# Kernel tuning notes

Hardware: AMD Instinct MI355X
Metric: run time of the kernel (lower is better)

Reference implementation:

```python
import jax, jax.numpy as jnp
import numpy as np

B, K = 16384, 32      # batch nodes, sampled neighbors per node
N, F, E = 1000000, 128, 128  # table size, feature_dim, embed_dim


def setup_inputs() -> dict:
    key = jax.random.key(0)
    k1, k2, k3 = jax.random.split(key, 3)
    id2feat = jax.random.normal(k1, (N, F), dtype=jnp.float32)
    # xavier_uniform for weight
    limit = float(np.sqrt(6.0 / (F + E)))
    weight = jax.random.uniform(k2, (F, E), dtype=jnp.float32, minval=-limit, maxval=limit)
    bias = jnp.zeros((E,), dtype=jnp.float32)
    neigh_idx = jax.random.randint(k3, (B, K), 0, N, dtype=jnp.int64)
    return {"id2feat": id2feat, "weight": weight, "bias": bias, "neigh_idx": neigh_idx}


def reference(id2feat, weight, bias, neigh_idx):
    # gather neighbor features: [B, K, F]
    feats = id2feat[neigh_idx]
    # linear transform then mean over neighbors (== mask.mm(embed_matrix))
    emb = jnp.einsum('bkf,fe->bke', feats, weight) + bias  # [B, K, E]
    return emb.mean(axis=1)  # [B, E]
```

## Files before the change

### kernel.cpp

```cpp
#include <hip/hip_runtime.h>


#define BATCH 16384
#define KNB   32
#define FDIM  128
#define EDIM  128
#define ROWS_PER_BLOCK 16
#define IDX_PITCH 33
#define A_PITCH  132

__global__ __launch_bounds__(256, 2)
void spa_agg_kernel(const float* __restrict__ id2feat,
                    const float* __restrict__ weight,
                    const float* __restrict__ bias,
                    const int* __restrict__ neigh_idx,
                    float* __restrict__ out) {
    __shared__ float sW[FDIM * EDIM];
    __shared__ float sA[ROWS_PER_BLOCK * A_PITCH];
    __shared__ int   sIdx[ROWS_PER_BLOCK * IDX_PITCH];

    const int tid = threadIdx.x;
    const int lb  = tid >> 4;
    const int fg  = tid & 15;
    const int b0  = blockIdx.x * ROWS_PER_BLOCK;

    {
        const int base = b0 * KNB;
        for (int i = tid; i < ROWS_PER_BLOCK * KNB; i += 256) {
            int r = i >> 5, c = i & 31;
            sIdx[r * IDX_PITCH + c] = neigh_idx[base + i];
        }
    }
    {
        for (int i = tid; i < (FDIM * EDIM) / 4; i += 256) {
            int f = i >> 5, e4 = i & 31;
            const float4 w = *(const float4*)(weight + (size_t)f * EDIM + e4 * 4);
            *(float4*)&sW[f * 128 + (e4 & 1) * 64 + (e4 >> 1) * 4] = w;
        }
    }
    __syncthreads();

    {
        float acc[8];
        #pragma unroll
        for (int j = 0; j < 8; ++j) acc[j] = 0.f;
        const int* ip = &sIdx[lb * IDX_PITCH];
        #pragma unroll 8
        for (int k = 0; k < KNB; ++k) {
            const int row = ip[k];
            const float4* rp = (const float4*)(id2feat + (size_t)row * FDIM + fg * 8);
            const float4 r0 = rp[0];
            const float4 r1 = rp[1];
            acc[0] += r0.x; acc[1] += r0.y; acc[2] += r0.z; acc[3] += r0.w;
            acc[4] += r1.x; acc[5] += r1.y; acc[6] += r1.z; acc[7] += r1.w;
        }
        float* ap = &sA[lb * A_PITCH + fg * 8];
        #pragma unroll
        for (int j = 0; j < 8; ++j) ap[j] = acc[j] * (1.f / 32.f);
    }
    __syncthreads();

    {
        const int e0 = fg * 8;
        float acc[8];
        #pragma unroll
        for (int j = 0; j < 8; ++j) acc[j] = bias[e0 + j];
        const float* arow = &sA[lb * A_PITCH];
        #pragma unroll 4
        for (int f = 0; f < FDIM; ++f) {
            const float a   = arow[f];
            const float4 w0 = *(const float4*)&sW[f * 128 + fg * 4];
            const float4 w1 = *(const float4*)&sW[f * 128 + 64 + fg * 4];
            acc[0] += a * w0.x; acc[1] += a * w0.y;
            acc[2] += a * w0.z; acc[3] += a * w0.w;
            acc[4] += a * w1.x; acc[5] += a * w1.y;
            acc[6] += a * w1.z; acc[7] += a * w1.w;
        }
        float* op = out + (size_t)(b0 + lb) * EDIM + e0;
        *(float4*)op       = make_float4(acc[0], acc[1], acc[2], acc[3]);
        *(float4*)(op + 4) = make_float4(acc[4], acc[5], acc[6], acc[7]);
    }
}

extern "C" void kernel_launch(void* const* d_in, const int* in_sizes, int n_in,
                              void* d_out, int out_size, void* d_ws, size_t ws_size,
                              hipStream_t stream) {
    const float* id2feat = (const float*)d_in[0];
    const float* weight  = (const float*)d_in[1];
    const float* bias    = (const float*)d_in[2];
    const int*   neigh   = (const int*)d_in[3];
    float*       outp    = (float*)d_out;

    dim3 grid(BATCH / ROWS_PER_BLOCK);
    dim3 block(256);
    spa_agg_kernel<<<grid, block, 0, stream>>>(id2feat, weight, bias, neigh, outp);
}
```

Before: 609.4 us.

## Drop shared weight staging and raise occupancy with 8 rows per block

Removes the 64KB shared-memory copy of the weight matrix and reads weights directly from global/L2 in the matvec phase, cutting LDS use so many more blocks fit per CU. Each warp now handles one batch row with 32 lanes each loading one float4 of a neighbor row, giving coalesced 512B gathers. Rows per block shrink to 8 and launch bounds rise to 6 blocks per SM to hide gather latency. The trade-off is that every block re-reads the 64KB weight from cache, which adds L2 traffic.

```diff
diff --git a/kernel.cpp b/kernel.cpp
--- a/kernel.cpp
+++ b/kernel.cpp
@@ -5,80 +5,58 @@
 #define KNB   32
 #define FDIM  128
 #define EDIM  128
-#define ROWS_PER_BLOCK 16
+#define ROWS_PER_BLOCK 8
 #define IDX_PITCH 33
 #define A_PITCH  132
 
-__global__ __launch_bounds__(256, 2)
+__global__ __launch_bounds__(256, 6)
 void spa_agg_kernel(const float* __restrict__ id2feat,
                     const float* __restrict__ weight,
                     const float* __restrict__ bias,
                     const int* __restrict__ neigh_idx,
                     float* __restrict__ out) {
-    __shared__ float sW[FDIM * EDIM];
     __shared__ float sA[ROWS_PER_BLOCK * A_PITCH];
     __shared__ int   sIdx[ROWS_PER_BLOCK * IDX_PITCH];
 
     const int tid = threadIdx.x;
-    const int lb  = tid >> 4;
-    const int fg  = tid & 15;
+    const int lb  = tid >> 5;
+    const int lr  = tid & 31;
     const int b0  = blockIdx.x * ROWS_PER_BLOCK;
 
     {
-        const int base = b0 * KNB;
-        for (int i = tid; i < ROWS_PER_BLOCK * KNB; i += 256) {
-            int r = i >> 5, c = i & 31;
-            sIdx[r * IDX_PITCH + c] = neigh_idx[base + i];
-        }
-    }
-    {
-        for (int i = tid; i < (FDIM * EDIM) / 4; i += 256) {
-            int f = i >> 5, e4 = i & 31;
-            const float4 w = *(const float4*)(weight + (size_t)f * EDIM + e4 * 4);
-            *(float4*)&sW[f * 128 + (e4 & 1) * 64 + (e4 >> 1) * 4] = w;
-        }
+        sIdx[lb * IDX_PITCH + lr] = neigh_idx[b0 * KNB + tid];
     }
     __syncthreads();
 
     {
-        float acc[8];
-        #pragma unroll
-        for (int j = 0; j < 8; ++j) acc[j] = 0.f;
+        float a0 = 0.f, a1 = 0.f, a2 = 0.f, a3 = 0.f;
         const int* ip = &sIdx[lb * IDX_PITCH];
+        const float* gbase = id2feat + lr * 4;
         #pragma unroll 8
         for (int k = 0; k < KNB; ++k) {
             const int row = ip[k];
-            const float4* rp = (const float4*)(id2feat + (size_t)row * FDIM + fg * 8);
-            const float4 r0 = rp[0];
-            const float4 r1 = rp[1];
-            acc[0] += r0.x; acc[1] += r0.y; acc[2] += r0.z; acc[3] += r0.w;
-            acc[4] += r1.x; acc[5] += r1.y; acc[6] += r1.z; acc[7] += r1.w;
+            const float4 r0 = *(const float4*)(gbase + (size_t)row * FDIM);
+            a0 += r0.x; a1 += r0.y; a2 += r0.z; a3 += r0.w;
         }
-        float* ap = &sA[lb * A_PITCH + fg * 8];
-        #pragma unroll
-        for (int j = 0; j < 8; ++j) ap[j] = acc[j] * (1.f / 32.f);
+        *(float4*)&sA[lb * A_PITCH + lr * 4] =
+            make_float4(a0 * (1.f / 32.f), a1 * (1.f / 32.f),
+                        a2 * (1.f / 32.f), a3 * (1.f / 32.f));
     }
     __syncthreads();
 
     {
-        const int e0 = fg * 8;
-        float acc[8];
-        #pragma unroll
-        for (int j = 0; j < 8; ++j) acc[j] = bias[e0 + j];
+        const int e0 = lr * 4;
+        float4 acc = *(const float4*)(bias + e0);
         const float* arow = &sA[lb * A_PITCH];
-        #pragma unroll 4
+        const float* wp = weight + e0;
+        #pragma unroll 8
         for (int f = 0; f < FDIM; ++f) {
-            const float a   = arow[f];
-            const float4 w0 = *(const float4*)&sW[f * 128 + fg * 4];
-            const float4 w1 = *(const float4*)&sW[f * 128 + 64 + fg * 4];
-            acc[0] += a * w0.x; acc[1] += a * w0.y;
-            acc[2] += a * w0.z; acc[3] += a * w0.w;
-            acc[4] += a * w1.x; acc[5] += a * w1.y;
-            acc[6] += a * w1.z; acc[7] += a * w1.w;
+            const float a  = arow[f];
+            const float4 w = *(const float4*)(wp + (size_t)f * EDIM);
+            acc.x += a * w.x; acc.y += a * w.y;
+            acc.z += a * w.z; acc.w += a * w.w;
         }
-        float* op = out + (size_t)(b0 + lb) * EDIM + e0;
-        *(float4*)op       = make_float4(acc[0], acc[1], acc[2], acc[3]);
-        *(float4*)(op + 4) = make_float4(acc[4], acc[5], acc[6], acc[7]);
+        *(float4*)(out + (size_t)(b0 + lb) * EDIM + e0) = acc;
     }
 }
 
```

Result: no change. 612.8 us (+0.6%).
